# Performance work log

Hardware: AMD Instinct MI355X
Metric: run time of the kernel (lower is better)

The kernel has to match this reference:

```python
import jax, jax.numpy as jnp
import numpy as np

B, S, HID, NH = 2, 2048, 1024, 16
HD = HID // NH
BASE = 10000.0


def _rope_tables(seq_len, head_dim):
    i = jnp.arange(0, head_dim, 2, dtype=jnp.float32)
    theta = BASE ** (-i / head_dim)
    pos = jnp.arange(seq_len, dtype=jnp.float32)
    m_theta = jnp.outer(pos, theta)  # [S, HD/2]
    cos = jnp.repeat(jnp.cos(m_theta), 2, axis=1)  # [S, HD]
    sin = jnp.repeat(jnp.sin(m_theta), 2, axis=1)
    return cos, sin


def _apply_rope(x, cos, sin):
    # x: [B, NH, S, HD]; interleaved rotation: (-x1, x0, -x3, x2, ...)
    x_even = x[..., 0::2]
    x_odd = x[..., 1::2]
    inv_x = jnp.stack((-x_odd, x_even), axis=-1).reshape(x.shape)
    return x * cos[None, None] + inv_x * sin[None, None]


def setup_inputs() -> dict:
    key = jax.random.key(0)
    ks = jax.random.split(key, 7)
    q = jax.random.normal(ks[0], (B, S, HID), dtype=jnp.float32)
    k = jax.random.normal(ks[1], (B, S, HID), dtype=jnp.float32)
    v = jax.random.normal(ks[2], (B, S, HID), dtype=jnp.float32)
    scale = 1.0 / np.sqrt(HID)
    Wq = jax.random.normal(ks[3], (HID, HID), dtype=jnp.float32) * scale
    Wk = jax.random.normal(ks[4], (HID, HID), dtype=jnp.float32) * scale
    Wv = jax.random.normal(ks[5], (HID, HID), dtype=jnp.float32) * scale
    Wo = jax.random.normal(ks[6], (HID, HID), dtype=jnp.float32) * scale
    mask = jnp.triu(jnp.ones((S, S), dtype=bool), k=1)[None, None]  # causal, True = masked
    return {"q": q, "k": k, "v": v, "mask": mask,
            "Wq": Wq, "Wk": Wk, "Wv": Wv, "Wo": Wo}


def reference(q, k, v, mask, Wq, Wk, Wv, Wo):
    cos, sin = _rope_tables(S, HD)
    # Linear (torch stores weight as [out, in]; y = x @ W.T)
    qh = (q @ Wq.T).reshape(B, S, NH, HD).transpose(0, 2, 1, 3)
    kh = (k @ Wk.T).reshape(B, S, NH, HD).transpose(0, 2, 1, 3)
    vh = (v @ Wv.T).reshape(B, S, NH, HD).transpose(0, 2, 1, 3)
    qh = _apply_rope(qh, cos, sin)
    kh = _apply_rope(kh, cos, sin)
    scores = jnp.einsum("bhqd,bhkd->bhqk", qh, kh) / np.sqrt(HD)
    neg_min = jnp.finfo(jnp.float32).min
    scores = jnp.where(mask, neg_min, scores)
    attn = jax.nn.softmax(scores, axis=-1)
    out = jnp.einsum("bhqk,bhkd->bhqd", attn, vh)  # [B,NH,S,HD]
    out = out.transpose(0, 2, 1, 3).reshape(B, S, HID)
    return out @ Wo.T
```

## Files before the change

### kernel.cpp

```cpp
#include <hip/hip_runtime.h>

#define S_LEN 2048
#define HIDN  1024
#define NHEAD 16
#define HDIM  64
#define MROWS 4096
#define KDIM  1024
#define NDIM  1024

typedef __attribute__((ext_vector_type(8))) short bf16x8;
typedef __attribute__((ext_vector_type(4))) short bf16x4;
typedef __attribute__((ext_vector_type(4))) float f32x4;

static __device__ __forceinline__ ushort f2bf(float f) {
    unsigned int u = __float_as_uint(f);
    u = (u + 0x7fffu + ((u >> 16) & 1u)) >> 16;
    return (ushort)u;
}
static __device__ __forceinline__ float bf2f(ushort u) {
    return __uint_as_float(((unsigned int)u) << 16);
}

static __device__ __forceinline__ void gload16(const ushort* g, ushort* l) {
    __builtin_amdgcn_global_load_lds(
        (const __attribute__((address_space(1))) unsigned int*)g,
        (__attribute__((address_space(3))) unsigned int*)l, 16, 0, 0);
}

__global__ __launch_bounds__(256) void prep_kernel(
    const float* __restrict__ q, const float* __restrict__ k,
    const float* __restrict__ v, const float* __restrict__ Wq,
    const float* __restrict__ Wk, const float* __restrict__ Wv,
    const float* __restrict__ Wo,
    ushort* __restrict__ qb, ushort* __restrict__ kb, ushort* __restrict__ vb,
    ushort* __restrict__ Wqb, ushort* __restrict__ Wkb, ushort* __restrict__ Wvb,
    ushort* __restrict__ Wob,
    float* __restrict__ rc, float* __restrict__ rs)
{
    const long Q4 = (long)MROWS * KDIM / 4;
    const long W4 = (long)NDIM * KDIM / 4;
    if (blockIdx.x < 16384) {
        long i = (long)blockIdx.x * 256 + threadIdx.x;
        const float* src; ushort* dst; long off;
        if (i < Q4)          { src = q; dst = qb; off = i; }
        else if (i < 2 * Q4) { src = k; dst = kb; off = i - Q4; }
        else if (i < 3 * Q4) { src = v; dst = vb; off = i - 2 * Q4; }
        else {
            long t = i - 3 * Q4;
            int wsel = (int)(t >> 18);
            off = t & (W4 - 1);
            src = (wsel == 0) ? Wq : (wsel == 1) ? Wk : (wsel == 2) ? Wv : Wo;
            dst = (wsel == 0) ? Wqb : (wsel == 1) ? Wkb : (wsel == 2) ? Wvb : Wob;
        }
        float4 vv = ((const float4*)src)[off];
        ushort4 o;
        o.x = f2bf(vv.x); o.y = f2bf(vv.y); o.z = f2bf(vv.z); o.w = f2bf(vv.w);
        ((ushort4*)dst)[off] = o;
    } else {
        int idx = (blockIdx.x - 16384) * 256 + threadIdx.x;
        int s  = idx >> 5;
        int jp = idx & 31;
        float theta = expf(-(float)(2 * jp) * (9.210340371976184f / 64.0f));
        float ang = (float)s * theta;
        float sv, cv;
        sincosf(ang, &sv, &cv);
        rc[idx] = cv;
        rs[idx] = sv;
    }
}

static __device__ __forceinline__ void gemm_mainloop128(
    const ushort* __restrict__ A, const ushort* __restrict__ W,
    ushort* As, ushort* Bs, f32x4 (&acc)[4][4],
    int m0, int n0, int tid)
{
    const int lane = tid & 63, wid = tid >> 6;
    const int wm = wid & 1, wn = wid >> 1;
    const int quad = lane >> 4, l15 = lane & 15;

    for (int k0 = 0; k0 < KDIM; k0 += 64) {
        __syncthreads();
#pragma unroll
        for (int rr = 0; rr < 4; ++rr) {
            int sidx = tid + rr * 256;
            int row = sidx >> 3;
            int g = (sidx & 7) ^ (row & 7);
            gload16(A + (size_t)(m0 + row) * KDIM + k0 + g * 8, As + sidx * 8);
            gload16(W + (size_t)(n0 + row) * KDIM + k0 + g * 8, Bs + sidx * 8);
        }
        __syncthreads();

#pragma unroll
        for (int ks = 0; ks < 2; ++ks) {
            bf16x8 af[4], bfr[4];
#pragma unroll
            for (int i = 0; i < 4; ++i) {
                int row = wm * 64 + i * 16 + l15;
                int gg = ((ks << 2) | quad) ^ (row & 7);
                af[i] = *(const bf16x8*)&As[row * 64 + gg * 8];
            }
#pragma unroll
            for (int j = 0; j < 4; ++j) {
                int row = wn * 64 + j * 16 + l15;
                int gg = ((ks << 2) | quad) ^ (row & 7);
                bfr[j] = *(const bf16x8*)&Bs[row * 64 + gg * 8];
            }
#pragma unroll
            for (int i = 0; i < 4; ++i)
#pragma unroll
                for (int j = 0; j < 4; ++j)
                    acc[i][j] = __builtin_amdgcn_mfma_f32_16x16x32_bf16(
                        af[i], bfr[j], acc[i][j], 0, 0, 0);
        }
    }
}

__global__ __launch_bounds__(256, 3) void gemm_qkv(
    const ushort* __restrict__ qb, const ushort* __restrict__ kb,
    const ushort* __restrict__ vb,
    const ushort* __restrict__ Wqb, const ushort* __restrict__ Wkb,
    const ushort* __restrict__ Wvb,
    ushort* __restrict__ Qh, ushort* __restrict__ Kh, ushort* __restrict__ Vt,
    const float* __restrict__ rc, const float* __restrict__ rs)
{
    __shared__ __align__(16) ushort As[128 * 64];
    __shared__ __align__(16) ushort Bs[128 * 64];

    const int tid = threadIdx.x;
    const int lane = tid & 63, wid = tid >> 6;
    const int wm = wid & 1, wn = wid >> 1;
    const int quad = lane >> 4, l15 = lane & 15;
    const int z = blockIdx.z;

    const ushort* A; const ushort* W; int m0, n0;
    if (z == 2) {
        m0 = (int)blockIdx.y * 128;
        n0 = (int)blockIdx.x * 128;
        A = Wvb; W = vb;
    } else {
        m0 = blockIdx.x * 128; n0 = blockIdx.y * 128;
        A = (z == 0) ? qb : kb;
        W = (z == 0) ? Wqb : Wkb;
    }

    f32x4 acc[4][4];
#pragma unroll
    for (int i = 0; i < 4; ++i)
#pragma unroll
        for (int j = 0; j < 4; ++j) acc[i][j] = 0.0f;

    gemm_mainloop128(A, W, As, Bs, acc, m0, n0, tid);

    if (z != 2) {
        ushort* out = (z == 0) ? Qh : Kh;
        const float scale = (z == 0) ? 0.18033688011112042f : 1.0f;
#pragma unroll
        for (int i = 0; i < 4; ++i)
#pragma unroll
            for (int j = 0; j < 4; ++j)
#pragma unroll
                for (int r = 0; r < 4; ++r) {
                    int m = m0 + wm * 64 + i * 16 + quad * 4 + r;
                    int n = n0 + wn * 64 + j * 16 + l15;
                    float v = acc[i][j][r];
                    int b = m >> 11, s = m & (S_LEN - 1);
                    int h = n >> 6, d = n & 63;
                    int pidx = s * 32 + (d >> 1);
                    float cv = rc[pidx], sv = rs[pidx];
                    float partner = __shfl_xor(v, 1);
                    v = (d & 1) ? (v * cv + partner * sv)
                                : (v * cv - partner * sv);
                    out[((size_t)((b * NHEAD + h) * S_LEN + s)) * HDIM + d] =
                        f2bf(v * scale);
                }
    } else {
#pragma unroll
        for (int i = 0; i < 4; ++i)
#pragma unroll
            for (int j = 0; j < 4; ++j)
#pragma unroll
                for (int r = 0; r < 4; ++r) {
                    int m = m0 + wm * 64 + i * 16 + quad * 4 + r;
                    int n = n0 + wn * 64 + j * 16 + l15;
                    int h = m >> 6, d = m & 63;
                    int b = n >> 11, s = n & (S_LEN - 1);
                    Vt[((size_t)((b * NHEAD + h) * HDIM + d)) * S_LEN + s] =
                        f2bf(acc[i][j][r]);
                }
    }
}

__global__ __launch_bounds__(256) void gemm_out(
    const ushort* __restrict__ O0, const ushort* __restrict__ O1,
    const float* __restrict__ L0, const float* __restrict__ L1,
    const ushort* __restrict__ W, float* __restrict__ out)
{
    __shared__ __align__(16) ushort As[64 * 64];
    __shared__ __align__(16) ushort Bs[128 * 64];

    const int tid = threadIdx.x;
    const int lane = tid & 63, wid = tid >> 6;
    const int wm = wid & 1, wn = wid >> 1;
    const int quad = lane >> 4, l15 = lane & 15;
    const int m0 = blockIdx.x * 64, n0 = blockIdx.y * 128;

    f32x4 acc[2][4];
#pragma unroll
    for (int i = 0; i < 2; ++i)
#pragma unroll
        for (int j = 0; j < 4; ++j) acc[i][j] = 0.0f;

    for (int k0 = 0; k0 < KDIM; k0 += 64) {
        const int h = k0 >> 6;
        bf16x8 a0[2], a1[2];
        float li[2];
#pragma unroll
        for (int rr = 0; rr < 2; ++rr) {
            int sidx = tid + rr * 256;
            int row = sidx >> 3;
            int g = (sidx & 7) ^ (row & 7);
            int m = m0 + row, bb = m >> 11, s = m & (S_LEN - 1);
            size_t rowO = (size_t)(bb * NHEAD + h) * S_LEN + s;
            a0[rr] = *(const bf16x8*)(O0 + rowO * HDIM + g * 8);
            a1[rr] = *(const bf16x8*)(O1 + rowO * HDIM + g * 8);
            li[rr] = __builtin_amdgcn_rcpf(L0[rowO] + L1[rowO]);
        }
        __syncthreads();
#pragma unroll
        for (int rr = 0; rr < 2; ++rr) {
            int sidx = tid + rr * 256;
            bf16x8 packed;
#pragma unroll
            for (int e = 0; e < 8; ++e) {
                float f = (bf2f((ushort)a0[rr][e]) + bf2f((ushort)a1[rr][e])) * li[rr];
                packed[e] = (short)(__float_as_uint(f) >> 16);
            }
            *(bf16x8*)&As[sidx * 8] = packed;
        }
#pragma unroll
        for (int rr = 0; rr < 4; ++rr) {
            int sidx = tid + rr * 256;
            int row = sidx >> 3;
            int g = (sidx & 7) ^ (row & 7);
            gload16(W + (size_t)(n0 + row) * KDIM + k0 + g * 8, Bs + sidx * 8);
        }
        __syncthreads();

#pragma unroll
        for (int ks = 0; ks < 2; ++ks) {
            bf16x8 af[2], bfr[4];
#pragma unroll
            for (int i = 0; i < 2; ++i) {
                int row = wm * 32 + i * 16 + l15;
                int gg = ((ks << 2) | quad) ^ (row & 7);
                af[i] = *(const bf16x8*)&As[row * 64 + gg * 8];
            }
#pragma unroll
            for (int j = 0; j < 4; ++j) {
                int row = wn * 64 + j * 16 + l15;
                int gg = ((ks << 2) | quad) ^ (row & 7);
                bfr[j] = *(const bf16x8*)&Bs[row * 64 + gg * 8];
            }
#pragma unroll
            for (int i = 0; i < 2; ++i)
#pragma unroll
                for (int j = 0; j < 4; ++j)
                    acc[i][j] = __builtin_amdgcn_mfma_f32_16x16x32_bf16(
                        af[i], bfr[j], acc[i][j], 0, 0, 0);
        }
    }

#pragma unroll
    for (int i = 0; i < 2; ++i)
#pragma unroll
        for (int j = 0; j < 4; ++j)
#pragma unroll
            for (int r = 0; r < 4; ++r) {
                int m = m0 + wm * 32 + i * 16 + quad * 4 + r;
                int n = n0 + wn * 64 + j * 16 + l15;
                out[(size_t)m * NDIM + n] = acc[i][j][r];
            }
}

__global__ __launch_bounds__(256) void attn_mfma(
    const ushort* __restrict__ Qh, const ushort* __restrict__ Kh,
    const ushort* __restrict__ Vt,
    ushort* __restrict__ O0, ushort* __restrict__ O1,
    float* __restrict__ L0, float* __restrict__ L1)
{
    __shared__ __align__(16) ushort Ks[64 * 64];
    __shared__ __align__(16) ushort Vs[64 * 64];

    const int tid = threadIdx.x;
    const int lane = tid & 63, w = tid >> 6;
    const int quad = lane >> 4, l15 = lane & 15;
    const int id = blockIdx.x;
    const int h = id & 15, b = (id >> 4) & 1, t = id >> 5;

    int seg, y;
    if (t < 32) { seg = (t & 1) ? 0 : 1; y = (t & 1) ? 31 - (t >> 1) : (t >> 1); }
    else { int u = t - 32; seg = (u & 1) ? 0 : 1;
           y = (u & 1) ? 15 - (u >> 1) : 16 + (u >> 1); }

    const int qt = seg ? (31 - y) : y;
    const int lo = seg ? ((33 - y) >> 1) : 0;
    const int hi = seg ? (32 - y) : ((y + 2) >> 1);
    const int q0 = qt * 64;
    const size_t hoff = (size_t)(b * NHEAD + h) * S_LEN * HDIM;

    bf16x8 qf[2];
#pragma unroll
    for (int ks = 0; ks < 2; ++ks)
        qf[ks] = *(const bf16x8*)(Qh + hoff +
            (size_t)(q0 + w * 16 + l15) * HDIM + ks * 32 + quad * 8);

    f32x4 Oa[4];
#pragma unroll
    for (int mt = 0; mt < 4; ++mt) Oa[mt] = 0.0f;
    float lsum = 0.f;
    const int myq = q0 + w * 16 + l15;

    const ushort* kg[2];
    const ushort* vgr[2];
    int vwa[2][2];
#pragma unroll
    for (int rr = 0; rr < 2; ++rr) {
        int sidx = tid + rr * 256;
        int row = sidx >> 3;
        int gsw = (sidx & 7) ^ (row & 7);
        kg[rr] = Kh + hoff + (size_t)(lo * 64 + row) * HDIM + gsw * 8;
        int sp = sidx & 7;
        vgr[rr] = Vt + hoff + (size_t)row * S_LEN + lo * 64 + sp * 8;
        vwa[rr][0] = row * 64 + ((2 * sp)     ^ (row & 15)) * 4;
        vwa[rr][1] = row * 64 + ((2 * sp + 1) ^ (row & 15)) * 4;
    }

    bf16x8 vv[2];
    if (lo < hi) {
#pragma unroll
        for (int rr = 0; rr < 2; ++rr) { vv[rr] = *(const bf16x8*)vgr[rr]; vgr[rr] += 64; }
    }

    for (int kt = lo; kt < hi; ++kt) {
        const int k0 = kt * 64;
        const bool diag = (kt == qt);
        __syncthreads();
#pragma unroll
        for (int rr = 0; rr < 2; ++rr) {
            *(bf16x4*)&Vs[vwa[rr][0]] =
                __builtin_shufflevector(vv[rr], vv[rr], 0, 1, 2, 3);
            *(bf16x4*)&Vs[vwa[rr][1]] =
                __builtin_shufflevector(vv[rr], vv[rr], 4, 5, 6, 7);
            gload16(kg[rr], Ks + (tid + rr * 256) * 8);
            kg[rr] += 64 * HDIM;
        }
        if (kt + 1 < hi) {
#pragma unroll
            for (int rr = 0; rr < 2; ++rr) { vv[rr] = *(const bf16x8*)vgr[rr]; vgr[rr] += 64; }
        }
        __syncthreads();

        f32x4 Sa[4];
#pragma unroll
        for (int jm = 0; jm < 4; ++jm) Sa[jm] = 0.0f;
#pragma unroll
        for (int ks = 0; ks < 2; ++ks) {
            const int p = ((ks << 2) | quad) ^ (l15 & 7);
            bf16x8 kf[4];
#pragma unroll
            for (int jm = 0; jm < 4; ++jm)
                kf[jm] = *(const bf16x8*)&Ks[(jm * 16 + l15) * 64 + p * 8];
#pragma unroll
            for (int jm = 0; jm < 4; ++jm)
                Sa[jm] = __builtin_amdgcn_mfma_f32_16x16x32_bf16(kf[jm], qf[ks],
                                                                 Sa[jm], 0, 0, 0);
        }

        bf16x4 pb[4];
#pragma unroll
        for (int jm = 0; jm < 4; ++jm) {
#pragma unroll
            for (int r = 0; r < 4; ++r) {
                float pv = __builtin_amdgcn_exp2f(Sa[jm][r]);
                if (diag) {
                    int key = k0 + jm * 16 + quad * 4 + r;
                    if (key > myq) pv = 0.f;
                }
                lsum += pv;
                pb[jm][r] = (short)(__float_as_uint(pv) >> 16);
            }
        }

#pragma unroll
        for (int jm = 0; jm < 4; ++jm) {
            const int slot = (((jm * 4 + quad) ^ l15) << 2);
#pragma unroll
            for (int mt = 0; mt < 4; ++mt) {
                bf16x4 vf = *(const bf16x4*)&Vs[(mt * 16 + l15) * 64 + slot];
                Oa[mt] = __builtin_amdgcn_mfma_f32_16x16x16bf16_1k(vf, pb[jm],
                                                                   Oa[mt], 0, 0, 0);
            }
        }
    }

    lsum += __shfl_xor(lsum, 16);
    lsum += __shfl_xor(lsum, 32);

    ushort* Op = seg ? O1 : O0;
    float*  Lp = seg ? L1 : L0;
    const size_t row = (size_t)(b * NHEAD + h) * S_LEN + myq;
#pragma unroll
    for (int mt = 0; mt < 4; ++mt) {
        ushort4 o;
        o.x = f2bf(Oa[mt][0]); o.y = f2bf(Oa[mt][1]);
        o.z = f2bf(Oa[mt][2]); o.w = f2bf(Oa[mt][3]);
        *(ushort4*)&Op[row * HDIM + mt * 16 + quad * 4] = o;
    }
    if (quad == 0) Lp[row] = lsum;
}

extern "C" void kernel_launch(void* const* d_in, const int* in_sizes, int n_in,
                              void* d_out, int out_size, void* d_ws, size_t ws_size,
                              hipStream_t stream) {
    const float* qf  = (const float*)d_in[0];
    const float* kf  = (const float*)d_in[1];
    const float* vf  = (const float*)d_in[2];
    const float* Wqf = (const float*)d_in[4];
    const float* Wkf = (const float*)d_in[5];
    const float* Wvf = (const float*)d_in[6];
    const float* Wof = (const float*)d_in[7];
    float* out = (float*)d_out;

    char* wsp = (char*)d_ws;
    float* rc = (float*)wsp;            wsp += 65536 * 4;
    float* rs = (float*)wsp;            wsp += 65536 * 4;
    ushort* qb  = (ushort*)wsp;         wsp += (size_t)MROWS * KDIM * 2;
    ushort* kb  = (ushort*)wsp;         wsp += (size_t)MROWS * KDIM * 2;
    ushort* vb  = (ushort*)wsp;         wsp += (size_t)MROWS * KDIM * 2;
    ushort* Wqb = (ushort*)wsp;         wsp += (size_t)NDIM * KDIM * 2;
    ushort* Wkb = (ushort*)wsp;         wsp += (size_t)NDIM * KDIM * 2;
    ushort* Wvb = (ushort*)wsp;         wsp += (size_t)NDIM * KDIM * 2;
    ushort* Wob = (ushort*)wsp;         wsp += (size_t)NDIM * KDIM * 2;
    ushort* Qh  = (ushort*)wsp;         wsp += (size_t)MROWS * HIDN * 2;
    ushort* Kh  = (ushort*)wsp;         wsp += (size_t)MROWS * HIDN * 2;
    ushort* Vt  = (ushort*)wsp;

    ushort* O0 = qb;
    ushort* O1 = kb;
    float*  L0 = (float*)vb;
    float*  L1 = (float*)vb + 65536;

    prep_kernel<<<16640, 256, 0, stream>>>(qf, kf, vf, Wqf, Wkf, Wvf, Wof,
                                           qb, kb, vb, Wqb, Wkb, Wvb, Wob, rc, rs);

    gemm_qkv<<<dim3(32, 8, 3), 256, 0, stream>>>(
        qb, kb, vb, Wqb, Wkb, Wvb, Qh, Kh, Vt, rc, rs);

    attn_mfma<<<2048, 256, 0, stream>>>(Qh, Kh, Vt, O0, O1, L0, L1);

    gemm_out<<<dim3(64, 8), 256, 0, stream>>>(O0, O1, L0, L1, Wob, out);
}
```

Measured before the change: 214.7 us.

## Process two query tiles per attention block to reuse K/V loads

Each attention workgroup now handles 128 query rows (two 64-row groups) against each staged K/V tile, halving the grid and the number of K/V shared-memory loads per query. The key range is split into two equal halves by seg, with a new scheduling of blocks over banks, and the causal mask check is done per 64-row group. Register pressure roughly doubles for accumulators, and launch bounds now request 4 blocks per CU, which may force spills or cut occupancy.

```diff
diff --git a/kernel.cpp b/kernel.cpp
--- a/kernel.cpp
+++ b/kernel.cpp
@@ -282,7 +282,7 @@
             }
 }
 
-__global__ __launch_bounds__(256) void attn_mfma(
+__global__ __launch_bounds__(256, 4) void attn_mfma(
     const ushort* __restrict__ Qh, const ushort* __restrict__ Kh,
     const ushort* __restrict__ Vt,
     ushort* __restrict__ O0, ushort* __restrict__ O1,
@@ -295,29 +295,33 @@
     const int lane = tid & 63, w = tid >> 6;
     const int quad = lane >> 4, l15 = lane & 15;
     const int id = blockIdx.x;
-    const int h = id & 15, b = (id >> 4) & 1, t = id >> 5;
-
-    int seg, y;
-    if (t < 32) { seg = (t & 1) ? 0 : 1; y = (t & 1) ? 31 - (t >> 1) : (t >> 1); }
-    else { int u = t - 32; seg = (u & 1) ? 0 : 1;
-           y = (u & 1) ? 15 - (u >> 1) : 16 + (u >> 1); }
-
-    const int qt = seg ? (31 - y) : y;
-    const int lo = seg ? ((33 - y) >> 1) : 0;
-    const int hi = seg ? (32 - y) : ((y + 2) >> 1);
-    const int q0 = qt * 64;
+    const int bank = id >> 8;
+    const int rrr  = id & 255;
+    const int qidx = rrr >> 5;
+    const int bh   = rrr & 31;
+    const int b = bh >> 4, h = bh & 15;
+    const int qt  = (bank < 2) ? (15 - qidx) : qidx;
+    const int seg = bank & 1;
+
+    const int lo = seg ? (qt + 1) : 0;
+    const int hi = lo + qt + 1;
+    const int q0 = qt * 128;
     const size_t hoff = (size_t)(b * NHEAD + h) * S_LEN * HDIM;
 
-    bf16x8 qf[2];
-#pragma unroll
-    for (int ks = 0; ks < 2; ++ks)
-        qf[ks] = *(const bf16x8*)(Qh + hoff +
-            (size_t)(q0 + w * 16 + l15) * HDIM + ks * 32 + quad * 8);
-
-    f32x4 Oa[4];
-#pragma unroll
-    for (int mt = 0; mt < 4; ++mt) Oa[mt] = 0.0f;
-    float lsum = 0.f;
+    bf16x8 qf[2][2];
+#pragma unroll
+    for (int g = 0; g < 2; ++g)
+#pragma unroll
+        for (int ks = 0; ks < 2; ++ks)
+            qf[g][ks] = *(const bf16x8*)(Qh + hoff +
+                (size_t)(q0 + g * 64 + w * 16 + l15) * HDIM + ks * 32 + quad * 8);
+
+    f32x4 Oa[2][4];
+#pragma unroll
+    for (int g = 0; g < 2; ++g)
+#pragma unroll
+        for (int mt = 0; mt < 4; ++mt) Oa[g][mt] = 0.0f;
+    float lsum0 = 0.f, lsum1 = 0.f;
     const int myq = q0 + w * 16 + l15;
 
     const ushort* kg[2];
@@ -336,14 +340,11 @@
     }
 
     bf16x8 vv[2];
-    if (lo < hi) {
-#pragma unroll
-        for (int rr = 0; rr < 2; ++rr) { vv[rr] = *(const bf16x8*)vgr[rr]; vgr[rr] += 64; }
-    }
+#pragma unroll
+    for (int rr = 0; rr < 2; ++rr) { vv[rr] = *(const bf16x8*)vgr[rr]; vgr[rr] += 64; }
 
     for (int kt = lo; kt < hi; ++kt) {
         const int k0 = kt * 64;
-        const bool diag = (kt == qt);
         __syncthreads();
 #pragma unroll
         for (int rr = 0; rr < 2; ++rr) {
@@ -360,9 +361,11 @@
         }
         __syncthreads();
 
-        f32x4 Sa[4];
-#pragma unroll
-        for (int jm = 0; jm < 4; ++jm) Sa[jm] = 0.0f;
+        f32x4 Sa[2][4];
+#pragma unroll
+        for (int g = 0; g < 2; ++g)
+#pragma unroll
+            for (int jm = 0; jm < 4; ++jm) Sa[g][jm] = 0.0f;
 #pragma unroll
         for (int ks = 0; ks < 2; ++ks) {
             const int p = ((ks << 2) | quad) ^ (l15 & 7);
@@ -371,23 +374,31 @@
             for (int jm = 0; jm < 4; ++jm)
                 kf[jm] = *(const bf16x8*)&Ks[(jm * 16 + l15) * 64 + p * 8];
 #pragma unroll
-            for (int jm = 0; jm < 4; ++jm)
-                Sa[jm] = __builtin_amdgcn_mfma_f32_16x16x32_bf16(kf[jm], qf[ks],
-                                                                 Sa[jm], 0, 0, 0);
-        }
-
-        bf16x4 pb[4];
-#pragma unroll
-        for (int jm = 0; jm < 4; ++jm) {
-#pragma unroll
-            for (int r = 0; r < 4; ++r) {
-                float pv = __builtin_amdgcn_exp2f(Sa[jm][r]);
-                if (diag) {
-                    int key = k0 + jm * 16 + quad * 4 + r;
-                    if (key > myq) pv = 0.f;
+            for (int jm = 0; jm < 4; ++jm) {
+                Sa[0][jm] = __builtin_amdgcn_mfma_f32_16x16x32_bf16(
+                    kf[jm], qf[0][ks], Sa[0][jm], 0, 0, 0);
+                Sa[1][jm] = __builtin_amdgcn_mfma_f32_16x16x32_bf16(
+                    kf[jm], qf[1][ks], Sa[1][jm], 0, 0, 0);
+            }
+        }
+
+        bf16x4 pb[2][4];
+#pragma unroll
+        for (int g = 0; g < 2; ++g) {
+            const bool dg = (k0 + 63 > q0 + g * 64 + w * 16);
+            const int mq = myq + g * 64;
+#pragma unroll
+            for (int jm = 0; jm < 4; ++jm) {
+#pragma unroll
+                for (int r = 0; r < 4; ++r) {
+                    float pv = __builtin_amdgcn_exp2f(Sa[g][jm][r]);
+                    if (dg) {
+                        int key = k0 + jm * 16 + quad * 4 + r;
+                        if (key > mq) pv = 0.f;
+                    }
+                    if (g == 0) lsum0 += pv; else lsum1 += pv;
+                    pb[g][jm][r] = (short)(__float_as_uint(pv) >> 16);
                 }
-                lsum += pv;
-                pb[jm][r] = (short)(__float_as_uint(pv) >> 16);
             }
         }
 
@@ -397,26 +408,34 @@
 #pragma unroll
             for (int mt = 0; mt < 4; ++mt) {
                 bf16x4 vf = *(const bf16x4*)&Vs[(mt * 16 + l15) * 64 + slot];
-                Oa[mt] = __builtin_amdgcn_mfma_f32_16x16x16bf16_1k(vf, pb[jm],
-                                                                   Oa[mt], 0, 0, 0);
-            }
-        }
-    }
-
-    lsum += __shfl_xor(lsum, 16);
-    lsum += __shfl_xor(lsum, 32);
+                Oa[0][mt] = __builtin_amdgcn_mfma_f32_16x16x16bf16_1k(
+                    vf, pb[0][jm], Oa[0][mt], 0, 0, 0);
+                Oa[1][mt] = __builtin_amdgcn_mfma_f32_16x16x16bf16_1k(
+                    vf, pb[1][jm], Oa[1][mt], 0, 0, 0);
+            }
+        }
+    }
+
+    lsum0 += __shfl_xor(lsum0, 16);
+    lsum0 += __shfl_xor(lsum0, 32);
+    lsum1 += __shfl_xor(lsum1, 16);
+    lsum1 += __shfl_xor(lsum1, 32);
 
     ushort* Op = seg ? O1 : O0;
     float*  Lp = seg ? L1 : L0;
-    const size_t row = (size_t)(b * NHEAD + h) * S_LEN + myq;
+    const size_t row0 = (size_t)(b * NHEAD + h) * S_LEN + myq;
+    const size_t row1 = row0 + 64;
 #pragma unroll
     for (int mt = 0; mt < 4; ++mt) {
-        ushort4 o;
-        o.x = f2bf(Oa[mt][0]); o.y = f2bf(Oa[mt][1]);
-        o.z = f2bf(Oa[mt][2]); o.w = f2bf(Oa[mt][3]);
-        *(ushort4*)&Op[row * HDIM + mt * 16 + quad * 4] = o;
-    }
-    if (quad == 0) Lp[row] = lsum;
+        ushort4 o0, o1;
+        o0.x = f2bf(Oa[0][mt][0]); o0.y = f2bf(Oa[0][mt][1]);
+        o0.z = f2bf(Oa[0][mt][2]); o0.w = f2bf(Oa[0][mt][3]);
+        o1.x = f2bf(Oa[1][mt][0]); o1.y = f2bf(Oa[1][mt][1]);
+        o1.z = f2bf(Oa[1][mt][2]); o1.w = f2bf(Oa[1][mt][3]);
+        *(ushort4*)&Op[row0 * HDIM + mt * 16 + quad * 4] = o0;
+        *(ushort4*)&Op[row1 * HDIM + mt * 16 + quad * 4] = o1;
+    }
+    if (quad == 0) { Lp[row0] = lsum0; Lp[row1] = lsum1; }
 }
 
 extern "C" void kernel_launch(void* const* d_in, const int* in_sizes, int n_in,
@@ -456,7 +475,7 @@
     gemm_qkv<<<dim3(32, 8, 3), 256, 0, stream>>>(
         qb, kb, vb, Wqb, Wkb, Wvb, Qh, Kh, Vt, rc, rs);
 
-    attn_mfma<<<2048, 256, 0, stream>>>(Qh, Kh, Vt, O0, O1, L0, L1);
+    attn_mfma<<<1024, 256, 0, stream>>>(Qh, Kh, Vt, O0, O1, L0, L1);
 
     gemm_out<<<dim3(64, 8), 256, 0, stream>>>(O0, O1, L0, L1, Wob, out);
 }
```

After: 213.7 us. No clear change (-0.5%).

## Make attention kernel persistent with atomic work-queue tile scheduling

Applied to the files above, without the earlier changes.

The attention kernel now launches 1024 persistent blocks. Each block repeatedly takes the next of the 2048 work items from a global atomic counter, which prep_kernel resets to zero. Items are handed out in the existing heavy-first ordering, so load balancing follows the order items are claimed rather than hardware block dispatch. The cost is an atomic plus an extra barrier per item, and the block can no longer rely on being freshly launched for each tile.

```diff
diff --git a/kernel.cpp b/kernel.cpp
--- a/kernel.cpp
+++ b/kernel.cpp
@@ -35,7 +35,7 @@
     ushort* __restrict__ qb, ushort* __restrict__ kb, ushort* __restrict__ vb,
     ushort* __restrict__ Wqb, ushort* __restrict__ Wkb, ushort* __restrict__ Wvb,
     ushort* __restrict__ Wob,
-    float* __restrict__ rc, float* __restrict__ rs)
+    float* __restrict__ rc, float* __restrict__ rs, int* __restrict__ ctr)
 {
     const long Q4 = (long)MROWS * KDIM / 4;
     const long W4 = (long)NDIM * KDIM / 4;
@@ -58,6 +58,7 @@
         ((ushort4*)dst)[off] = o;
     } else {
         int idx = (blockIdx.x - 16384) * 256 + threadIdx.x;
+        if (idx == 0) *ctr = 0;
         int s  = idx >> 5;
         int jp = idx & 31;
         float theta = expf(-(float)(2 * jp) * (9.210340371976184f / 64.0f));
@@ -286,137 +287,150 @@
     const ushort* __restrict__ Qh, const ushort* __restrict__ Kh,
     const ushort* __restrict__ Vt,
     ushort* __restrict__ O0, ushort* __restrict__ O1,
-    float* __restrict__ L0, float* __restrict__ L1)
+    float* __restrict__ L0, float* __restrict__ L1,
+    int* __restrict__ ctr)
 {
     __shared__ __align__(16) ushort Ks[64 * 64];
     __shared__ __align__(16) ushort Vs[64 * 64];
+    __shared__ int s_id;
 
     const int tid = threadIdx.x;
     const int lane = tid & 63, w = tid >> 6;
     const int quad = lane >> 4, l15 = lane & 15;
-    const int id = blockIdx.x;
-    const int h = id & 15, b = (id >> 4) & 1, t = id >> 5;
-
-    int seg, y;
-    if (t < 32) { seg = (t & 1) ? 0 : 1; y = (t & 1) ? 31 - (t >> 1) : (t >> 1); }
-    else { int u = t - 32; seg = (u & 1) ? 0 : 1;
-           y = (u & 1) ? 15 - (u >> 1) : 16 + (u >> 1); }
-
-    const int qt = seg ? (31 - y) : y;
-    const int lo = seg ? ((33 - y) >> 1) : 0;
-    const int hi = seg ? (32 - y) : ((y + 2) >> 1);
-    const int q0 = qt * 64;
-    const size_t hoff = (size_t)(b * NHEAD + h) * S_LEN * HDIM;
-
-    bf16x8 qf[2];
-#pragma unroll
-    for (int ks = 0; ks < 2; ++ks)
-        qf[ks] = *(const bf16x8*)(Qh + hoff +
-            (size_t)(q0 + w * 16 + l15) * HDIM + ks * 32 + quad * 8);
-
-    f32x4 Oa[4];
-#pragma unroll
-    for (int mt = 0; mt < 4; ++mt) Oa[mt] = 0.0f;
-    float lsum = 0.f;
-    const int myq = q0 + w * 16 + l15;
-
-    const ushort* kg[2];
-    const ushort* vgr[2];
-    int vwa[2][2];
+
+    int krow[2], kgsw[2], vsp[2], vwa[2][2];
 #pragma unroll
     for (int rr = 0; rr < 2; ++rr) {
         int sidx = tid + rr * 256;
         int row = sidx >> 3;
-        int gsw = (sidx & 7) ^ (row & 7);
-        kg[rr] = Kh + hoff + (size_t)(lo * 64 + row) * HDIM + gsw * 8;
-        int sp = sidx & 7;
-        vgr[rr] = Vt + hoff + (size_t)row * S_LEN + lo * 64 + sp * 8;
-        vwa[rr][0] = row * 64 + ((2 * sp)     ^ (row & 15)) * 4;
-        vwa[rr][1] = row * 64 + ((2 * sp + 1) ^ (row & 15)) * 4;
-    }
-
-    bf16x8 vv[2];
-    if (lo < hi) {
-#pragma unroll
-        for (int rr = 0; rr < 2; ++rr) { vv[rr] = *(const bf16x8*)vgr[rr]; vgr[rr] += 64; }
-    }
-
-    for (int kt = lo; kt < hi; ++kt) {
-        const int k0 = kt * 64;
-        const bool diag = (kt == qt);
+        krow[rr] = row;
+        kgsw[rr] = (sidx & 7) ^ (row & 7);
+        vsp[rr]  = sidx & 7;
+        vwa[rr][0] = row * 64 + ((2 * vsp[rr])     ^ (row & 15)) * 4;
+        vwa[rr][1] = row * 64 + ((2 * vsp[rr] + 1) ^ (row & 15)) * 4;
+    }
+
+    for (;;) {
+        if (tid == 0) s_id = atomicAdd(ctr, 1);
         __syncthreads();
+        const int id = s_id;
+        if (id >= 2048) break;
+
+        const int h = id & 15, b = (id >> 4) & 1, t = id >> 5;
+
+        int seg, y;
+        if (t < 32) { seg = (t & 1) ? 0 : 1; y = (t & 1) ? 31 - (t >> 1) : (t >> 1); }
+        else { int u = t - 32; seg = (u & 1) ? 0 : 1;
+               y = (u & 1) ? 15 - (u >> 1) : 16 + (u >> 1); }
+
+        const int qt = seg ? (31 - y) : y;
+        const int lo = seg ? ((33 - y) >> 1) : 0;
+        const int hi = seg ? (32 - y) : ((y + 2) >> 1);
+        const int q0 = qt * 64;
+        const size_t hoff = (size_t)(b * NHEAD + h) * S_LEN * HDIM;
+
+        bf16x8 qf[2];
+#pragma unroll
+        for (int ks = 0; ks < 2; ++ks)
+            qf[ks] = *(const bf16x8*)(Qh + hoff +
+                (size_t)(q0 + w * 16 + l15) * HDIM + ks * 32 + quad * 8);
+
+        f32x4 Oa[4];
+#pragma unroll
+        for (int mt = 0; mt < 4; ++mt) Oa[mt] = 0.0f;
+        float lsum = 0.f;
+        const int myq = q0 + w * 16 + l15;
+
+        const ushort* kg[2]; const ushort* vgr[2];
 #pragma unroll
         for (int rr = 0; rr < 2; ++rr) {
-            *(bf16x4*)&Vs[vwa[rr][0]] =
-                __builtin_shufflevector(vv[rr], vv[rr], 0, 1, 2, 3);
-            *(bf16x4*)&Vs[vwa[rr][1]] =
-                __builtin_shufflevector(vv[rr], vv[rr], 4, 5, 6, 7);
-            gload16(kg[rr], Ks + (tid + rr * 256) * 8);
-            kg[rr] += 64 * HDIM;
-        }
-        if (kt + 1 < hi) {
+            kg[rr]  = Kh + hoff + (size_t)(lo * 64 + krow[rr]) * HDIM + kgsw[rr] * 8;
+            vgr[rr] = Vt + hoff + (size_t)krow[rr] * S_LEN + lo * 64 + vsp[rr] * 8;
+        }
+
+        bf16x8 vv[2];
+        if (lo < hi) {
 #pragma unroll
             for (int rr = 0; rr < 2; ++rr) { vv[rr] = *(const bf16x8*)vgr[rr]; vgr[rr] += 64; }
         }
-        __syncthreads();
-
-        f32x4 Sa[4];
-#pragma unroll
-        for (int jm = 0; jm < 4; ++jm) Sa[jm] = 0.0f;
-#pragma unroll
-        for (int ks = 0; ks < 2; ++ks) {
-            const int p = ((ks << 2) | quad) ^ (l15 & 7);
-            bf16x8 kf[4];
-#pragma unroll
-            for (int jm = 0; jm < 4; ++jm)
-                kf[jm] = *(const bf16x8*)&Ks[(jm * 16 + l15) * 64 + p * 8];
-#pragma unroll
-            for (int jm = 0; jm < 4; ++jm)
-                Sa[jm] = __builtin_amdgcn_mfma_f32_16x16x32_bf16(kf[jm], qf[ks],
-                                                                 Sa[jm], 0, 0, 0);
-        }
-
-        bf16x4 pb[4];
-#pragma unroll
-        for (int jm = 0; jm < 4; ++jm) {
-#pragma unroll
-            for (int r = 0; r < 4; ++r) {
-                float pv = __builtin_amdgcn_exp2f(Sa[jm][r]);
-                if (diag) {
-                    int key = k0 + jm * 16 + quad * 4 + r;
-                    if (key > myq) pv = 0.f;
+
+        for (int kt = lo; kt < hi; ++kt) {
+            const int k0 = kt * 64;
+            const bool diag = (kt == qt);
+            __syncthreads();
+#pragma unroll
+            for (int rr = 0; rr < 2; ++rr) {
+                *(bf16x4*)&Vs[vwa[rr][0]] =
+                    __builtin_shufflevector(vv[rr], vv[rr], 0, 1, 2, 3);
+                *(bf16x4*)&Vs[vwa[rr][1]] =
+                    __builtin_shufflevector(vv[rr], vv[rr], 4, 5, 6, 7);
+                gload16(kg[rr], Ks + (tid + rr * 256) * 8);
+                kg[rr] += 64 * HDIM;
+            }
+            if (kt + 1 < hi) {
+#pragma unroll
+                for (int rr = 0; rr < 2; ++rr) { vv[rr] = *(const bf16x8*)vgr[rr]; vgr[rr] += 64; }
+            }
+            __syncthreads();
+
+            f32x4 Sa[4];
+#pragma unroll
+            for (int jm = 0; jm < 4; ++jm) Sa[jm] = 0.0f;
+#pragma unroll
+            for (int ks = 0; ks < 2; ++ks) {
+                const int p = ((ks << 2) | quad) ^ (l15 & 7);
+                bf16x8 kf[4];
+#pragma unroll
+                for (int jm = 0; jm < 4; ++jm)
+                    kf[jm] = *(const bf16x8*)&Ks[(jm * 16 + l15) * 64 + p * 8];
+#pragma unroll
+                for (int jm = 0; jm < 4; ++jm)
+                    Sa[jm] = __builtin_amdgcn_mfma_f32_16x16x32_bf16(
+                        kf[jm], qf[ks], Sa[jm], 0, 0, 0);
+            }
+
+            bf16x4 pb[4];
+#pragma unroll
+            for (int jm = 0; jm < 4; ++jm) {
+#pragma unroll
+                for (int r = 0; r < 4; ++r) {
+                    float pv = __builtin_amdgcn_exp2f(Sa[jm][r]);
+                    if (diag) {
+                        int key = k0 + jm * 16 + quad * 4 + r;
+                        if (key > myq) pv = 0.f;
+                    }
+                    lsum += pv;
+                    pb[jm][r] = (short)(__float_as_uint(pv) >> 16);
                 }
-                lsum += pv;
-                pb[jm][r] = (short)(__float_as_uint(pv) >> 16);
-            }
-        }
-
-#pragma unroll
-        for (int jm = 0; jm < 4; ++jm) {
-            const int slot = (((jm * 4 + quad) ^ l15) << 2);
-#pragma unroll
-            for (int mt = 0; mt < 4; ++mt) {
-                bf16x4 vf = *(const bf16x4*)&Vs[(mt * 16 + l15) * 64 + slot];
-                Oa[mt] = __builtin_amdgcn_mfma_f32_16x16x16bf16_1k(vf, pb[jm],
-                                                                   Oa[mt], 0, 0, 0);
-            }
-        }
-    }
-
-    lsum += __shfl_xor(lsum, 16);
-    lsum += __shfl_xor(lsum, 32);
-
-    ushort* Op = seg ? O1 : O0;
-    float*  Lp = seg ? L1 : L0;
-    const size_t row = (size_t)(b * NHEAD + h) * S_LEN + myq;
-#pragma unroll
-    for (int mt = 0; mt < 4; ++mt) {
-        ushort4 o;
-        o.x = f2bf(Oa[mt][0]); o.y = f2bf(Oa[mt][1]);
-        o.z = f2bf(Oa[mt][2]); o.w = f2bf(Oa[mt][3]);
-        *(ushort4*)&Op[row * HDIM + mt * 16 + quad * 4] = o;
-    }
-    if (quad == 0) Lp[row] = lsum;
+            }
+
+#pragma unroll
+            for (int jm = 0; jm < 4; ++jm) {
+                const int slot = (((jm * 4 + quad) ^ l15) << 2);
+#pragma unroll
+                for (int mt = 0; mt < 4; ++mt) {
+                    bf16x4 vf = *(const bf16x4*)&Vs[(mt * 16 + l15) * 64 + slot];
+                    Oa[mt] = __builtin_amdgcn_mfma_f32_16x16x16bf16_1k(
+                        vf, pb[jm], Oa[mt], 0, 0, 0);
+                }
+            }
+        }
+
+        lsum += __shfl_xor(lsum, 16);
+        lsum += __shfl_xor(lsum, 32);
+
+        ushort* Op = seg ? O1 : O0;
+        float*  Lp = seg ? L1 : L0;
+        const size_t row = (size_t)(b * NHEAD + h) * S_LEN + myq;
+#pragma unroll
+        for (int mt = 0; mt < 4; ++mt) {
+            ushort4 o;
+            o.x = f2bf(Oa[mt][0]); o.y = f2bf(Oa[mt][1]);
+            o.z = f2bf(Oa[mt][2]); o.w = f2bf(Oa[mt][3]);
+            *(ushort4*)&Op[row * HDIM + mt * 16 + quad * 4] = o;
+        }
+        if (quad == 0) Lp[row] = lsum;
+    }
 }
 
 extern "C" void kernel_launch(void* const* d_in, const int* in_sizes, int n_in,
@@ -432,6 +446,7 @@
     float* out = (float*)d_out;
 
     char* wsp = (char*)d_ws;
+    int* ctr = (int*)wsp;               wsp += 256;
     float* rc = (float*)wsp;            wsp += 65536 * 4;
     float* rs = (float*)wsp;            wsp += 65536 * 4;
     ushort* qb  = (ushort*)wsp;         wsp += (size_t)MROWS * KDIM * 2;
@@ -451,12 +466,13 @@
     float*  L1 = (float*)vb + 65536;
 
     prep_kernel<<<16640, 256, 0, stream>>>(qf, kf, vf, Wqf, Wkf, Wvf, Wof,
-                                           qb, kb, vb, Wqb, Wkb, Wvb, Wob, rc, rs);
+                                           qb, kb, vb, Wqb, Wkb, Wvb, Wob,
+                                           rc, rs, ctr);
 
     gemm_qkv<<<dim3(32, 8, 3), 256, 0, stream>>>(
         qb, kb, vb, Wqb, Wkb, Wvb, Qh, Kh, Vt, rc, rs);
 
-    attn_mfma<<<2048, 256, 0, stream>>>(Qh, Kh, Vt, O0, O1, L0, L1);
+    attn_mfma<<<1024, 256, 0, stream>>>(Qh, Kh, Vt, O0, O1, L0, L1, ctr);
 
     gemm_out<<<dim3(64, 8), 256, 0, stream>>>(O0, O1, L0, L1, Wob, out);
 }
```

Result: slower. 230.2 us (+7.2%).
